# Kernel tuning notes

Hardware: AMD Instinct MI355X
Metric: run time of the kernel (lower is better)

## Reference

```python
import jax, jax.numpy as jnp
import numpy as np

ENC_DIM, DEC_DIM, ATT_DIM = 2048, 512, 512
B, N = 256, 196


def setup_inputs() -> dict:
    key = jax.random.key(0)
    ks = jax.random.split(key, 8)
    s_enc = 1.0 / np.sqrt(ENC_DIM)
    s_dec = 1.0 / np.sqrt(DEC_DIM)
    s_full = 1.0 / np.sqrt(ATT_DIM)
    return {
        "encoder_out": jax.random.normal(ks[0], (B, N, ENC_DIM), jnp.float32),
        "hidden": jax.random.normal(ks[1], (B, DEC_DIM), jnp.float32),
        "W_enc": jax.random.uniform(ks[2], (ENC_DIM, ATT_DIM), jnp.float32, -s_enc, s_enc),
        "b_enc": jax.random.uniform(ks[3], (ATT_DIM,), jnp.float32, -s_enc, s_enc),
        "W_dec": jax.random.uniform(ks[4], (DEC_DIM, ATT_DIM), jnp.float32, -s_dec, s_dec),
        "b_dec": jax.random.uniform(ks[5], (ATT_DIM,), jnp.float32, -s_dec, s_dec),
        "W_full": jax.random.uniform(ks[6], (ATT_DIM, 1), jnp.float32, -s_full, s_full),
        "b_full": jax.random.uniform(ks[7], (1,), jnp.float32, -s_full, s_full),
    }


def reference(encoder_out, hidden, W_enc, b_enc, W_dec, b_dec, W_full, b_full):
    # enc proj: [B, N, A]; dec proj: [B, 1, A] broadcast over pixels
    att1 = jnp.einsum('bne,ea->bna', encoder_out, W_enc) + b_enc
    att2 = hidden @ W_dec + b_dec                       # [B, A]
    att = jax.nn.relu(att1 + att2[:, None, :])          # [B, N, A]
    scores = (jnp.einsum('bna,a->bn', att, W_full[:, 0]) + b_full[0])  # [B, N]
    alpha = jax.nn.softmax(scores, axis=1)              # softmax over pixels
    context = jnp.einsum('bne,bn->be', encoder_out, alpha)  # [B, E]
    return (context, alpha)
```

## Files before the change

### kernel.cpp

```cpp
#include <hip/hip_runtime.h>
#include <hip/hip_bf16.h>
#include <stdint.h>

#define ENC_DIM 2048
#define ATT_DIM 512
#define BATCH   256
#define NPIX    196
#define MTOT    (BATCH*NPIX)
#define CTX_OFF (BATCH*ENC_DIM)

typedef __attribute__((ext_vector_type(8))) short  short8;
typedef __attribute__((ext_vector_type(4))) float  f32x4;

__device__ __forceinline__ unsigned short f2bf(float x) {
    union { float f; uint32_t u; } v; v.f = x;
    return (unsigned short)((v.u + 0x7FFFu + ((v.u >> 16) & 1u)) >> 16);
}

__global__ __launch_bounds__(256) void pack_wenc(const float* __restrict__ W,
                                                 unsigned short* __restrict__ Wp) {
    const int i  = blockIdx.x * 256 + threadIdx.x;
    const int n  = i & 511;
    const int kg = i >> 9;
    short8 v;
#pragma unroll
    for (int j = 0; j < 8; ++j)
        v[j] = (short)f2bf(W[(size_t)(kg * 8 + j) * 512 + n]);
    *(short8*)(Wp + (size_t)i * 8) = v;
}

__global__ __launch_bounds__(256) void att2_kernel(const float* __restrict__ hidden,
                                                   const float* __restrict__ Wdec,
                                                   const float* __restrict__ bdec,
                                                   const float* __restrict__ benc,
                                                   float* __restrict__ att2p) {
    __shared__ float h[512];
    const int b   = blockIdx.x;
    const int tid = threadIdx.x;
    h[tid]       = hidden[(size_t)b * 512 + tid];
    h[tid + 256] = hidden[(size_t)b * 512 + tid + 256];
    __syncthreads();
    float acc0 = bdec[tid]       + benc[tid];
    float acc1 = bdec[tid + 256] + benc[tid + 256];
#pragma unroll 4
    for (int k = 0; k < 512; ++k) {
        const float hk = h[k];
        acc0 = fmaf(hk, Wdec[(size_t)k * 512 + tid],       acc0);
        acc1 = fmaf(hk, Wdec[(size_t)k * 512 + tid + 256], acc1);
    }
    att2p[(size_t)b * 512 + tid]       = acc0;
    att2p[(size_t)b * 512 + tid + 256] = acc1;
}

__global__ __launch_bounds__(512) void score_kernel(const float* __restrict__ enc,
                                                    const unsigned short* __restrict__ Wp,
                                                    const float* __restrict__ att2p,
                                                    const float* __restrict__ Wfull,
                                                    float* __restrict__ scores) {
    __shared__ __align__(16) unsigned short ldsA[64 * 64];
    __shared__ __align__(16) unsigned short ldsB[8 * 512 * 8];
    __shared__ float lds_att2[2][ATT_DIM];
    __shared__ float lds_wf[ATT_DIM];
    __shared__ float lds_sc[64];

    const int tid = threadIdx.x;
    const int w   = tid >> 6;
    const int l   = tid & 63;
    const int m0  = blockIdx.x * 64;
    const int b0  = m0 / NPIX;
    const int b1  = (m0 + 63) / NPIX;

    lds_att2[0][tid] = att2p[(size_t)b0 * ATT_DIM + tid];
    lds_att2[1][tid] = att2p[(size_t)b1 * ATT_DIM + tid];
    if (tid < ATT_DIM - 512 + 512) lds_wf[tid] = Wfull[tid];
    if (tid < 64) lds_sc[tid] = 0.0f;

    f32x4 acc[4][4];
#pragma unroll
    for (int i = 0; i < 4; ++i)
#pragma unroll
        for (int j = 0; j < 4; ++j)
            acc[i][j] = (f32x4){0.f, 0.f, 0.f, 0.f};

    const int ar      = tid >> 3;
    const int akk     = (tid & 7) << 3;
    const int aslot   = (tid & 7) ^ (ar & 7);
    unsigned short* aw = ldsA + ar * 64 + aslot * 8;
    const float* abase = enc + (size_t)(m0 + ar) * ENC_DIM + akk;

    const short8* bsrc = (const short8*)Wp;
    short8*       bdst = (short8*)ldsB;

    for (int kc = 0; kc < ENC_DIM; kc += 64) {
        f32x4 f0 = *(const f32x4*)(abase + kc);
        f32x4 f1 = *(const f32x4*)(abase + kc + 4);
        short8 av;
        av[0] = (short)f2bf(f0[0]); av[1] = (short)f2bf(f0[1]);
        av[2] = (short)f2bf(f0[2]); av[3] = (short)f2bf(f0[3]);
        av[4] = (short)f2bf(f1[0]); av[5] = (short)f2bf(f1[1]);
        av[6] = (short)f2bf(f1[2]); av[7] = (short)f2bf(f1[3]);
        *(short8*)aw = av;
        const short8* bs = bsrc + (size_t)kc * 64;
#pragma unroll
        for (int it = 0; it < 8; ++it)
            bdst[it * 512 + tid] = bs[it * 512 + tid];
        __syncthreads();
#pragma unroll
        for (int ks = 0; ks < 2; ++ks) {
            const int kg = ks * 4 + (l >> 4);
            short8 af[4], bfv[4];
#pragma unroll
            for (int mf = 0; mf < 4; ++mf) {
                const int r = mf * 16 + (l & 15);
                af[mf] = *(const short8*)(ldsA + r * 64 + ((kg ^ (r & 7)) * 8));
            }
#pragma unroll
            for (int nf = 0; nf < 4; ++nf) {
                const int col = w * 64 + nf * 16 + (l & 15);
                bfv[nf] = *(const short8*)(ldsB + ((size_t)kg * 512 + col) * 8);
            }
#pragma unroll
            for (int mf = 0; mf < 4; ++mf)
#pragma unroll
                for (int nf = 0; nf < 4; ++nf)
                    acc[mf][nf] = __builtin_amdgcn_mfma_f32_16x16x32_bf16(
                        af[mf], bfv[nf], acc[mf][nf], 0, 0, 0);
        }
        __syncthreads();
    }

#pragma unroll
    for (int mf = 0; mf < 4; ++mf) {
#pragma unroll
        for (int reg = 0; reg < 4; ++reg) {
            const int row = mf * 16 + ((l >> 4) << 2) + reg;
            const int sel = ((m0 + row) >= (b0 + 1) * NPIX) ? 1 : 0;
            float sv = 0.0f;
#pragma unroll
            for (int nf = 0; nf < 4; ++nf) {
                const int col = (w << 6) + (nf << 4) + (l & 15);
                float v = acc[mf][nf][reg] + lds_att2[sel][col];
                v = fmaxf(v, 0.0f);
                sv = fmaf(v, lds_wf[col], sv);
            }
            sv += __shfl_xor(sv, 8);
            sv += __shfl_xor(sv, 4);
            sv += __shfl_xor(sv, 2);
            sv += __shfl_xor(sv, 1);
            if ((l & 15) == 0) atomicAdd(&lds_sc[row], sv);
        }
    }
    __syncthreads();
    if (tid < 64) scores[m0 + tid] = lds_sc[tid];
}

__global__ __launch_bounds__(256) void ctx_kernel(const float* __restrict__ enc,
                                                  const float* __restrict__ scores,
                                                  float* __restrict__ out) {
    __shared__ float salpha[NPIX];
    __shared__ float red[8];
    const int tid  = threadIdx.x;
    const int lane = tid & 63;
    const int wid  = tid >> 6;
    const int b    = blockIdx.x >> 1;
    const int eh   = blockIdx.x & 1;

    const float sv = (tid < NPIX) ? scores[(size_t)b * NPIX + tid] : -1e30f;
    float mx = sv;
#pragma unroll
    for (int m = 32; m >= 1; m >>= 1) mx = fmaxf(mx, __shfl_xor(mx, m));
    if (lane == 0) red[wid] = mx;
    __syncthreads();
    if (tid == 0) red[4] = fmaxf(fmaxf(red[0], red[1]), fmaxf(red[2], red[3]));
    __syncthreads();
    const float bm = red[4];
    const float ex = (tid < NPIX) ? __expf(sv - bm) : 0.0f;
    float sm = ex;
#pragma unroll
    for (int m = 32; m >= 1; m >>= 1) sm += __shfl_xor(sm, m);
    if (lane == 0) red[wid] = sm;
    __syncthreads();
    if (tid == 0) red[5] = red[0] + red[1] + red[2] + red[3];
    __syncthreads();
    const float inv = 1.0f / red[5];
    const float av  = ex * inv;
    if (tid < NPIX) {
        salpha[tid] = av;
        if (eh == 0) out[CTX_OFF + (size_t)b * NPIX + tid] = av;
    }
    __syncthreads();

    const float* ep = enc + (size_t)b * NPIX * ENC_DIM + eh * 1024 + tid;
    float a0 = 0.f, a1 = 0.f, a2 = 0.f, a3 = 0.f;
#pragma unroll 2
    for (int n = 0; n < NPIX; ++n) {
        const float al = salpha[n];
        const float* p = ep + (size_t)n * ENC_DIM;
        a0 = fmaf(al, p[0],   a0);
        a1 = fmaf(al, p[256], a1);
        a2 = fmaf(al, p[512], a2);
        a3 = fmaf(al, p[768], a3);
    }
    float* cp = out + (size_t)b * 2048 + eh * 1024 + tid;
    cp[0]   = a0;
    cp[256] = a1;
    cp[512] = a2;
    cp[768] = a3;
}

extern "C" void kernel_launch(void* const* d_in, const int* in_sizes, int n_in,
                              void* d_out, int out_size, void* d_ws, size_t ws_size,
                              hipStream_t stream) {
    const float* enc    = (const float*)d_in[0];
    const float* hidden = (const float*)d_in[1];
    const float* Wenc   = (const float*)d_in[2];
    const float* benc   = (const float*)d_in[3];
    const float* Wdec   = (const float*)d_in[4];
    const float* bdec   = (const float*)d_in[5];
    const float* Wfull  = (const float*)d_in[6];
    float* out = (float*)d_out;

    unsigned short* Wp    = (unsigned short*)d_ws;
    float*          att2p = (float*)((char*)d_ws + (2u << 20));
    float*          scores= (float*)((char*)d_ws + (2u << 20) + (512u << 10));

    pack_wenc  <<<512, 256, 0, stream>>>(Wenc, Wp);
    att2_kernel<<<BATCH, 256, 0, stream>>>(hidden, Wdec, bdec, benc, att2p);
    score_kernel<<<MTOT / 64, 512, 0, stream>>>(enc, Wp, att2p, Wfull, scores);
    ctx_kernel <<<BATCH * 2, 256, 0, stream>>>(enc, scores, out);
}
```

Baseline: 303.1 us.

## Double-buffer score GEMM with direct global-to-LDS loads and vectorize context kernel

The score GEMM now uses a K-chunk of 32 with double-buffered LDS tiles. W_enc tiles are loaded with global_load_lds directly into shared memory, and the next chunk of encoder data is prefetched while the current one runs on MFMA, so there is one barrier per chunk instead of two. The context kernel splits each batch into four 512-wide slices, uses float4 loads, and has two pixel phases reduced through LDS. Halving K per step doubles the number of barriers and iterations, and the launch_bounds hint of 4 blocks may force register spills.

```diff
diff --git a/kernel.cpp b/kernel.cpp
--- a/kernel.cpp
+++ b/kernel.cpp
@@ -8,13 +8,21 @@
 #define NPIX    196
 #define MTOT    (BATCH*NPIX)
 #define CTX_OFF (BATCH*ENC_DIM)
+#define KC      32
+#define NCHUNK  (ENC_DIM/KC)
 
 typedef __attribute__((ext_vector_type(8))) short  short8;
 typedef __attribute__((ext_vector_type(4))) float  f32x4;
 
-__device__ __forceinline__ unsigned short f2bf(float x) {
+__device__ __forceinline__ unsigned int f2bf(float x) {
     union { float f; uint32_t u; } v; v.f = x;
-    return (unsigned short)((v.u + 0x7FFFu + ((v.u >> 16) & 1u)) >> 16);
+    return (v.u + 0x7FFFu + ((v.u >> 16) & 1u)) >> 16;
+}
+
+__device__ __forceinline__ void gll16(const void* g, void* l) {
+    __builtin_amdgcn_global_load_lds(
+        (const __attribute__((address_space(1))) unsigned int*)g,
+        (__attribute__((address_space(3))) unsigned int*)l, 16, 0, 0);
 }
 
 __global__ __launch_bounds__(256) void pack_wenc(const float* __restrict__ W,
@@ -52,13 +60,13 @@
     att2p[(size_t)b * 512 + tid + 256] = acc1;
 }
 
-__global__ __launch_bounds__(512) void score_kernel(const float* __restrict__ enc,
-                                                    const unsigned short* __restrict__ Wp,
-                                                    const float* __restrict__ att2p,
-                                                    const float* __restrict__ Wfull,
-                                                    float* __restrict__ scores) {
-    __shared__ __align__(16) unsigned short ldsA[64 * 64];
-    __shared__ __align__(16) unsigned short ldsB[8 * 512 * 8];
+__global__ __launch_bounds__(512, 4) void score_kernel(const float* __restrict__ enc,
+                                                       const unsigned short* __restrict__ Wp,
+                                                       const float* __restrict__ att2p,
+                                                       const float* __restrict__ Wfull,
+                                                       float* __restrict__ scores) {
+    __shared__ __align__(16) unsigned short ldsA[2][64 * KC];
+    __shared__ __align__(16) unsigned short ldsB[2][4 * 512 * 8];
     __shared__ float lds_att2[2][ATT_DIM];
     __shared__ float lds_wf[ATT_DIM];
     __shared__ float lds_sc[64];
@@ -72,7 +80,7 @@
 
     lds_att2[0][tid] = att2p[(size_t)b0 * ATT_DIM + tid];
     lds_att2[1][tid] = att2p[(size_t)b1 * ATT_DIM + tid];
-    if (tid < ATT_DIM - 512 + 512) lds_wf[tid] = Wfull[tid];
+    lds_wf[tid] = Wfull[tid];
     if (tid < 64) lds_sc[tid] = 0.0f;
 
     f32x4 acc[4][4];
@@ -82,51 +90,81 @@
         for (int j = 0; j < 4; ++j)
             acc[i][j] = (f32x4){0.f, 0.f, 0.f, 0.f};
 
-    const int ar      = tid >> 3;
-    const int akk     = (tid & 7) << 3;
-    const int aslot   = (tid & 7) ^ (ar & 7);
-    unsigned short* aw = ldsA + ar * 64 + aslot * 8;
-    const float* abase = enc + (size_t)(m0 + ar) * ENC_DIM + akk;
-
-    const short8* bsrc = (const short8*)Wp;
-    short8*       bdst = (short8*)ldsB;
-
-    for (int kc = 0; kc < ENC_DIM; kc += 64) {
-        f32x4 f0 = *(const f32x4*)(abase + kc);
-        f32x4 f1 = *(const f32x4*)(abase + kc + 4);
-        short8 av;
-        av[0] = (short)f2bf(f0[0]); av[1] = (short)f2bf(f0[1]);
-        av[2] = (short)f2bf(f0[2]); av[3] = (short)f2bf(f0[3]);
-        av[4] = (short)f2bf(f1[0]); av[5] = (short)f2bf(f1[1]);
-        av[6] = (short)f2bf(f1[2]); av[7] = (short)f2bf(f1[3]);
-        *(short8*)aw = av;
-        const short8* bs = bsrc + (size_t)kc * 64;
-#pragma unroll
-        for (int it = 0; it < 8; ++it)
-            bdst[it * 512 + tid] = bs[it * 512 + tid];
-        __syncthreads();
-#pragma unroll
-        for (int ks = 0; ks < 2; ++ks) {
-            const int kg = ks * 4 + (l >> 4);
-            short8 af[4], bfv[4];
-#pragma unroll
-            for (int mf = 0; mf < 4; ++mf) {
-                const int r = mf * 16 + (l & 15);
-                af[mf] = *(const short8*)(ldsA + r * 64 + ((kg ^ (r & 7)) * 8));
-            }
-#pragma unroll
-            for (int nf = 0; nf < 4; ++nf) {
-                const int col = w * 64 + nf * 16 + (l & 15);
-                bfv[nf] = *(const short8*)(ldsB + ((size_t)kg * 512 + col) * 8);
-            }
-#pragma unroll
-            for (int mf = 0; mf < 4; ++mf)
-#pragma unroll
-                for (int nf = 0; nf < 4; ++nf)
-                    acc[mf][nf] = __builtin_amdgcn_mfma_f32_16x16x32_bf16(
-                        af[mf], bfv[nf], acc[mf][nf], 0, 0, 0);
+    const int ar  = tid >> 3;
+    const int ah  = tid & 7;
+    const int axr = (ar >> 1) & 3;
+    const float* aG = enc + (size_t)(m0 + ar) * ENC_DIM + ah * 4;
+    const int a_wr_off = ar * KC + ((ah >> 1) ^ axr) * 8 + (ah & 1) * 4;
+
+    const unsigned char* WpB = (const unsigned char*)Wp;
+
+    int a_rd[4], b_rd[4];
+#pragma unroll
+    for (int mf = 0; mf < 4; ++mf) {
+        const int r = mf * 16 + (l & 15);
+        a_rd[mf] = r * KC + (((l >> 4) ^ ((r >> 1) & 3)) * 8);
+    }
+#pragma unroll
+    for (int nf = 0; nf < 4; ++nf) {
+        const int col = w * 64 + nf * 16 + (l & 15);
+        b_rd[nf] = ((l >> 4) * 512 + col) * 8;
+    }
+
+#pragma unroll
+    for (int it = 0; it < 4; ++it) {
+        const int seg = w * 4 + it;
+        gll16(WpB + (size_t)seg * 1024 + l * 16,
+              (unsigned char*)ldsB[0] + seg * 1024 + l * 16);
+    }
+    {
+        f32x4 a0 = *(const f32x4*)aG;
+        uint32_t* dst = (uint32_t*)(ldsA[0] + a_wr_off);
+        dst[0] = f2bf(a0[0]) | (f2bf(a0[1]) << 16);
+        dst[1] = f2bf(a0[2]) | (f2bf(a0[3]) << 16);
+    }
+    __syncthreads();
+
+#pragma unroll 2
+    for (int c = 0; c < NCHUNK - 1; ++c) {
+        const int p = c & 1;
+#pragma unroll
+        for (int it = 0; it < 4; ++it) {
+            const int seg = w * 4 + it;
+            gll16(WpB + (size_t)(c + 1) * 32768 + seg * 1024 + l * 16,
+                  (unsigned char*)ldsB[p ^ 1] + seg * 1024 + l * 16);
+        }
+        f32x4 an = *(const f32x4*)(aG + (c + 1) * KC);
+        short8 af[4], bfv[4];
+#pragma unroll
+        for (int mf = 0; mf < 4; ++mf) af[mf]  = *(const short8*)(ldsA[p] + a_rd[mf]);
+#pragma unroll
+        for (int nf = 0; nf < 4; ++nf) bfv[nf] = *(const short8*)(ldsB[p] + b_rd[nf]);
+#pragma unroll
+        for (int mf = 0; mf < 4; ++mf)
+#pragma unroll
+            for (int nf = 0; nf < 4; ++nf)
+                acc[mf][nf] = __builtin_amdgcn_mfma_f32_16x16x32_bf16(
+                    af[mf], bfv[nf], acc[mf][nf], 0, 0, 0);
+        {
+            uint32_t* dst = (uint32_t*)(ldsA[p ^ 1] + a_wr_off);
+            dst[0] = f2bf(an[0]) | (f2bf(an[1]) << 16);
+            dst[1] = f2bf(an[2]) | (f2bf(an[3]) << 16);
         }
         __syncthreads();
+    }
+    {
+        const int p = (NCHUNK - 1) & 1;
+        short8 af[4], bfv[4];
+#pragma unroll
+        for (int mf = 0; mf < 4; ++mf) af[mf]  = *(const short8*)(ldsA[p] + a_rd[mf]);
+#pragma unroll
+        for (int nf = 0; nf < 4; ++nf) bfv[nf] = *(const short8*)(ldsB[p] + b_rd[nf]);
+#pragma unroll
+        for (int mf = 0; mf < 4; ++mf)
+#pragma unroll
+            for (int nf = 0; nf < 4; ++nf)
+                acc[mf][nf] = __builtin_amdgcn_mfma_f32_16x16x32_bf16(
+                    af[mf], bfv[nf], acc[mf][nf], 0, 0, 0);
     }
 
 #pragma unroll
@@ -159,11 +197,12 @@
                                                   float* __restrict__ out) {
     __shared__ float salpha[NPIX];
     __shared__ float red[8];
+    __shared__ float partial[512];
     const int tid  = threadIdx.x;
     const int lane = tid & 63;
     const int wid  = tid >> 6;
-    const int b    = blockIdx.x >> 1;
-    const int eh   = blockIdx.x & 1;
+    const int b    = blockIdx.x >> 2;
+    const int eq   = blockIdx.x & 3;
 
     const float sv = (tid < NPIX) ? scores[(size_t)b * NPIX + tid] : -1e30f;
     float mx = sv;
@@ -183,29 +222,29 @@
     if (tid == 0) red[5] = red[0] + red[1] + red[2] + red[3];
     __syncthreads();
     const float inv = 1.0f / red[5];
-    const float av  = ex * inv;
     if (tid < NPIX) {
+        const float av = ex * inv;
         salpha[tid] = av;
-        if (eh == 0) out[CTX_OFF + (size_t)b * NPIX + tid] = av;
-    }
-    __syncthreads();
-
-    const float* ep = enc + (size_t)b * NPIX * ENC_DIM + eh * 1024 + tid;
-    float a0 = 0.f, a1 = 0.f, a2 = 0.f, a3 = 0.f;
-#pragma unroll 2
-    for (int n = 0; n < NPIX; ++n) {
+        if (eq == 0) out[CTX_OFF + (size_t)b * NPIX + tid] = av;
+    }
+    __syncthreads();
+
+    const int l128 = tid & 127;
+    const int ph   = tid >> 7;
+    const float* ep = enc + (size_t)b * NPIX * ENC_DIM + eq * 512 + l128 * 4;
+    f32x4 acc = (f32x4){0.f, 0.f, 0.f, 0.f};
+#pragma unroll 4
+    for (int n = ph; n < NPIX; n += 2) {
         const float al = salpha[n];
-        const float* p = ep + (size_t)n * ENC_DIM;
-        a0 = fmaf(al, p[0],   a0);
-        a1 = fmaf(al, p[256], a1);
-        a2 = fmaf(al, p[512], a2);
-        a3 = fmaf(al, p[768], a3);
-    }
-    float* cp = out + (size_t)b * 2048 + eh * 1024 + tid;
-    cp[0]   = a0;
-    cp[256] = a1;
-    cp[512] = a2;
-    cp[768] = a3;
+        f32x4 v = *(const f32x4*)(ep + (size_t)n * ENC_DIM);
+        acc += v * al;
+    }
+    if (ph == 1) *(f32x4*)(partial + l128 * 4) = acc;
+    __syncthreads();
+    if (ph == 0) {
+        f32x4 o = acc + *(const f32x4*)(partial + l128 * 4);
+        *(f32x4*)(out + (size_t)b * ENC_DIM + eq * 512 + l128 * 4) = o;
+    }
 }
 
 extern "C" void kernel_launch(void* const* d_in, const int* in_sizes, int n_in,
@@ -227,5 +266,5 @@
     pack_wenc  <<<512, 256, 0, stream>>>(Wenc, Wp);
     att2_kernel<<<BATCH, 256, 0, stream>>>(hidden, Wdec, bdec, benc, att2p);
     score_kernel<<<MTOT / 64, 512, 0, stream>>>(enc, Wp, att2p, Wfull, scores);
-    ctx_kernel <<<BATCH * 2, 256, 0, stream>>>(enc, scores, out);
-}
+    ctx_kernel <<<BATCH * 4, 256, 0, stream>>>(enc, scores, out);
+}
```

Result: slower. 335.6 us (+10.7%).

## Fuse score GEMM, softmax and context into one per-batch kernel

Applied to the files above, without the earlier changes.

Replaces the separate score and context kernels with one kernel per batch element. It computes the 196 pixel scores in two 112-row sub-tiles, using double-buffered bf16 A tiles in LDS and B fragments read directly from global/L2, then does the softmax and the context reduction in the same block. This is meant to drop the scores round trip and a kernel launch, and to reuse encoder_out while it is likely still in cache. In exchange the grid shrinks to 256 blocks, which may underfill the GPU, and padded rows waste some MFMA work.

```diff
diff --git a/kernel.cpp b/kernel.cpp
--- a/kernel.cpp
+++ b/kernel.cpp
@@ -6,15 +6,19 @@
 #define ATT_DIM 512
 #define BATCH   256
 #define NPIX    196
-#define MTOT    (BATCH*NPIX)
+#define MROWS   (BATCH*NPIX)
 #define CTX_OFF (BATCH*ENC_DIM)
+#define KC      128
+#define NCH     (ENC_DIM/KC)
+#define MSUB    112
+#define ABUF    (MSUB*KC*2)
 
 typedef __attribute__((ext_vector_type(8))) short  short8;
 typedef __attribute__((ext_vector_type(4))) float  f32x4;
 
-__device__ __forceinline__ unsigned short f2bf(float x) {
+__device__ __forceinline__ uint32_t f2bf(float x) {
     union { float f; uint32_t u; } v; v.f = x;
-    return (unsigned short)((v.u + 0x7FFFu + ((v.u >> 16) & 1u)) >> 16);
+    return (v.u + 0x7FFFu + ((v.u >> 16) & 1u)) >> 16;
 }
 
 __global__ __launch_bounds__(256) void pack_wenc(const float* __restrict__ W,
@@ -52,160 +56,190 @@
     att2p[(size_t)b * 512 + tid + 256] = acc1;
 }
 
-__global__ __launch_bounds__(512) void score_kernel(const float* __restrict__ enc,
-                                                    const unsigned short* __restrict__ Wp,
-                                                    const float* __restrict__ att2p,
-                                                    const float* __restrict__ Wfull,
-                                                    float* __restrict__ scores) {
-    __shared__ __align__(16) unsigned short ldsA[64 * 64];
-    __shared__ __align__(16) unsigned short ldsB[8 * 512 * 8];
-    __shared__ float lds_att2[2][ATT_DIM];
+__global__ __launch_bounds__(512, 2) void fused_kernel(const float* __restrict__ enc,
+                                                       const unsigned short* __restrict__ Wp,
+                                                       const float* __restrict__ att2p,
+                                                       const float* __restrict__ Wfull,
+                                                       float* __restrict__ out) {
+    __shared__ __align__(16) unsigned char ldsA[2 * ABUF];
+    __shared__ float lds_att2[ATT_DIM];
     __shared__ float lds_wf[ATT_DIM];
-    __shared__ float lds_sc[64];
+    __shared__ float lds_sc[224];
+    __shared__ float salpha[NPIX];
+    __shared__ float red[16];
 
     const int tid = threadIdx.x;
     const int w   = tid >> 6;
     const int l   = tid & 63;
-    const int m0  = blockIdx.x * 64;
-    const int b0  = m0 / NPIX;
-    const int b1  = (m0 + 63) / NPIX;
-
-    lds_att2[0][tid] = att2p[(size_t)b0 * ATT_DIM + tid];
-    lds_att2[1][tid] = att2p[(size_t)b1 * ATT_DIM + tid];
-    if (tid < ATT_DIM - 512 + 512) lds_wf[tid] = Wfull[tid];
-    if (tid < 64) lds_sc[tid] = 0.0f;
-
-    f32x4 acc[4][4];
-#pragma unroll
-    for (int i = 0; i < 4; ++i)
-#pragma unroll
-        for (int j = 0; j < 4; ++j)
-            acc[i][j] = (f32x4){0.f, 0.f, 0.f, 0.f};
-
-    const int ar      = tid >> 3;
-    const int akk     = (tid & 7) << 3;
-    const int aslot   = (tid & 7) ^ (ar & 7);
-    unsigned short* aw = ldsA + ar * 64 + aslot * 8;
-    const float* abase = enc + (size_t)(m0 + ar) * ENC_DIM + akk;
-
-    const short8* bsrc = (const short8*)Wp;
-    short8*       bdst = (short8*)ldsB;
-
-    for (int kc = 0; kc < ENC_DIM; kc += 64) {
-        f32x4 f0 = *(const f32x4*)(abase + kc);
-        f32x4 f1 = *(const f32x4*)(abase + kc + 4);
-        short8 av;
-        av[0] = (short)f2bf(f0[0]); av[1] = (short)f2bf(f0[1]);
-        av[2] = (short)f2bf(f0[2]); av[3] = (short)f2bf(f0[3]);
-        av[4] = (short)f2bf(f1[0]); av[5] = (short)f2bf(f1[1]);
-        av[6] = (short)f2bf(f1[2]); av[7] = (short)f2bf(f1[3]);
-        *(short8*)aw = av;
-        const short8* bs = bsrc + (size_t)kc * 64;
-#pragma unroll
-        for (int it = 0; it < 8; ++it)
-            bdst[it * 512 + tid] = bs[it * 512 + tid];
+    const int b   = blockIdx.x;
+
+    lds_att2[tid] = att2p[(size_t)b * ATT_DIM + tid];
+    lds_wf[tid]   = Wfull[tid];
+    if (tid < 224) lds_sc[tid] = 0.0f;
+
+    int boff[4];
+#pragma unroll
+    for (int nf = 0; nf < 4; ++nf)
+        boff[nf] = (((l >> 4) * 512) + (w << 6) + (nf << 4) + (l & 15)) * 8;
+
+    const int g  = tid & 31;
+    const int rr = tid >> 5;
+    const int aoffL0 = rr * 256 + (((g >> 1) ^ (rr & 7)) << 4) + ((g & 1) << 3);
+    const int axk   = l & 7;
+    const int afrow = (l & 15) << 8;
+
+    for (int sub = 0; sub < 2; ++sub) {
+        int rowOff[7];
+#pragma unroll
+        for (int i = 0; i < 7; ++i) {
+            int grow = b * NPIX + sub * MSUB + rr + 16 * i;
+            if (grow > MROWS - 1) grow = MROWS - 1;
+            rowOff[i] = grow * ENC_DIM;
+        }
+        const float* aBase = enc + g * 4;
+
+        f32x4 acc[7][4];
+#pragma unroll
+        for (int i = 0; i < 7; ++i)
+#pragma unroll
+            for (int j = 0; j < 4; ++j)
+                acc[i][j] = (f32x4){0.f, 0.f, 0.f, 0.f};
+
+        {
+            f32x4 sA[7];
+#pragma unroll
+            for (int i = 0; i < 7; ++i) sA[i] = *(const f32x4*)(aBase + rowOff[i]);
+#pragma unroll
+            for (int i = 0; i < 7; ++i) {
+                uint2 u;
+                u.x = f2bf(sA[i][0]) | (f2bf(sA[i][1]) << 16);
+                u.y = f2bf(sA[i][2]) | (f2bf(sA[i][3]) << 16);
+                *(uint2*)(ldsA + aoffL0 + i * 4096) = u;
+            }
+        }
         __syncthreads();
-#pragma unroll
-        for (int ks = 0; ks < 2; ++ks) {
-            const int kg = ks * 4 + (l >> 4);
-            short8 af[4], bfv[4];
-#pragma unroll
-            for (int mf = 0; mf < 4; ++mf) {
-                const int r = mf * 16 + (l & 15);
-                af[mf] = *(const short8*)(ldsA + r * 64 + ((kg ^ (r & 7)) * 8));
-            }
-#pragma unroll
-            for (int nf = 0; nf < 4; ++nf) {
-                const int col = w * 64 + nf * 16 + (l & 15);
-                bfv[nf] = *(const short8*)(ldsB + ((size_t)kg * 512 + col) * 8);
-            }
-#pragma unroll
-            for (int mf = 0; mf < 4; ++mf)
+
+        for (int c = 0; c < NCH; ++c) {
+            const int p = c & 1;
+            const unsigned char* ldsR = ldsA + p * ABUF;
+            unsigned char*       ldsW = ldsA + (p ^ 1) * ABUF;
+            const bool more = (c < NCH - 1);
+
+            f32x4 sA[7];
+            if (more) {
+#pragma unroll
+                for (int i = 0; i < 7; ++i)
+                    sA[i] = *(const f32x4*)(aBase + rowOff[i] + (c + 1) * KC);
+            }
+
+            const unsigned short* bC = Wp + (size_t)c * 65536;
+            short8 bf0[8], bf1[8];
+#pragma unroll
+            for (int s2 = 0; s2 < 2; ++s2)
 #pragma unroll
                 for (int nf = 0; nf < 4; ++nf)
-                    acc[mf][nf] = __builtin_amdgcn_mfma_f32_16x16x32_bf16(
-                        af[mf], bfv[nf], acc[mf][nf], 0, 0, 0);
-        }
-        __syncthreads();
-    }
-
-#pragma unroll
-    for (int mf = 0; mf < 4; ++mf) {
-#pragma unroll
-        for (int reg = 0; reg < 4; ++reg) {
-            const int row = mf * 16 + ((l >> 4) << 2) + reg;
-            const int sel = ((m0 + row) >= (b0 + 1) * NPIX) ? 1 : 0;
-            float sv = 0.0f;
-#pragma unroll
-            for (int nf = 0; nf < 4; ++nf) {
-                const int col = (w << 6) + (nf << 4) + (l & 15);
-                float v = acc[mf][nf][reg] + lds_att2[sel][col];
-                v = fmaxf(v, 0.0f);
-                sv = fmaf(v, lds_wf[col], sv);
-            }
-            sv += __shfl_xor(sv, 8);
-            sv += __shfl_xor(sv, 4);
-            sv += __shfl_xor(sv, 2);
-            sv += __shfl_xor(sv, 1);
-            if ((l & 15) == 0) atomicAdd(&lds_sc[row], sv);
-        }
-    }
-    __syncthreads();
-    if (tid < 64) scores[m0 + tid] = lds_sc[tid];
-}
-
-__global__ __launch_bounds__(256) void ctx_kernel(const float* __restrict__ enc,
-                                                  const float* __restrict__ scores,
-                                                  float* __restrict__ out) {
-    __shared__ float salpha[NPIX];
-    __shared__ float red[8];
-    const int tid  = threadIdx.x;
-    const int lane = tid & 63;
-    const int wid  = tid >> 6;
-    const int b    = blockIdx.x >> 1;
-    const int eh   = blockIdx.x & 1;
-
-    const float sv = (tid < NPIX) ? scores[(size_t)b * NPIX + tid] : -1e30f;
-    float mx = sv;
+                    bf0[s2 * 4 + nf] = *(const short8*)(bC + boff[nf] + s2 * 16384);
+
+#define STEP(S, BARR, BASE)                                                        \
+            {                                                                      \
+                const int so = ((((S) * 4) + (l >> 4)) ^ axk) << 4;                \
+                _Pragma("unroll")                                                  \
+                for (int mf = 0; mf < 7; ++mf) {                                   \
+                    short8 af = *(const short8*)(ldsR + afrow + so + mf * 4096);   \
+                    _Pragma("unroll")                                              \
+                    for (int nf = 0; nf < 4; ++nf)                                 \
+                        acc[mf][nf] = __builtin_amdgcn_mfma_f32_16x16x32_bf16(     \
+                            af, BARR[(BASE) + nf], acc[mf][nf], 0, 0, 0);          \
+                }                                                                  \
+            }
+
+            STEP(0, bf0, 0)
+#pragma unroll
+            for (int s2 = 0; s2 < 2; ++s2)
+#pragma unroll
+                for (int nf = 0; nf < 4; ++nf)
+                    bf1[s2 * 4 + nf] = *(const short8*)(bC + boff[nf] + (2 + s2) * 16384);
+            STEP(1, bf0, 4)
+            STEP(2, bf1, 0)
+            STEP(3, bf1, 4)
+#undef STEP
+
+            if (more) {
+#pragma unroll
+                for (int i = 0; i < 7; ++i) {
+                    uint2 u;
+                    u.x = f2bf(sA[i][0]) | (f2bf(sA[i][1]) << 16);
+                    u.y = f2bf(sA[i][2]) | (f2bf(sA[i][3]) << 16);
+                    *(uint2*)(ldsW + aoffL0 + i * 4096) = u;
+                }
+            }
+            __syncthreads();
+        }
+
+#pragma unroll
+        for (int mf = 0; mf < 7; ++mf) {
+#pragma unroll
+            for (int reg = 0; reg < 4; ++reg) {
+                const int row = sub * MSUB + mf * 16 + ((l >> 4) << 2) + reg;
+                float sv = 0.0f;
+#pragma unroll
+                for (int nf = 0; nf < 4; ++nf) {
+                    const int col = (w << 6) + (nf << 4) + (l & 15);
+                    float v = acc[mf][nf][reg] + lds_att2[col];
+                    v = fmaxf(v, 0.0f);
+                    sv = fmaf(v, lds_wf[col], sv);
+                }
+                sv += __shfl_xor(sv, 8);
+                sv += __shfl_xor(sv, 4);
+                sv += __shfl_xor(sv, 2);
+                sv += __shfl_xor(sv, 1);
+                if ((l & 15) == 0 && row < NPIX) atomicAdd(&lds_sc[row], sv);
+            }
+        }
+    }
+    __syncthreads();
+
+    const float sval = (tid < NPIX) ? lds_sc[tid] : -1e30f;
+    float mx = sval;
 #pragma unroll
     for (int m = 32; m >= 1; m >>= 1) mx = fmaxf(mx, __shfl_xor(mx, m));
-    if (lane == 0) red[wid] = mx;
-    __syncthreads();
-    if (tid == 0) red[4] = fmaxf(fmaxf(red[0], red[1]), fmaxf(red[2], red[3]));
-    __syncthreads();
-    const float bm = red[4];
-    const float ex = (tid < NPIX) ? __expf(sv - bm) : 0.0f;
+    if (l == 0) red[w] = mx;
+    __syncthreads();
+    if (tid == 0) {
+        float m2 = red[0];
+#pragma unroll
+        for (int i = 1; i < 8; ++i) m2 = fmaxf(m2, red[i]);
+        red[8] = m2;
+    }
+    __syncthreads();
+    const float bm = red[8];
+    const float ex = (tid < NPIX) ? __expf(sval - bm) : 0.0f;
     float sm = ex;
 #pragma unroll
     for (int m = 32; m >= 1; m >>= 1) sm += __shfl_xor(sm, m);
-    if (lane == 0) red[wid] = sm;
-    __syncthreads();
-    if (tid == 0) red[5] = red[0] + red[1] + red[2] + red[3];
-    __syncthreads();
-    const float inv = 1.0f / red[5];
-    const float av  = ex * inv;
+    if (l == 0) red[w] = sm;
+    __syncthreads();
+    if (tid == 0) {
+        float s2 = 0.f;
+#pragma unroll
+        for (int i = 0; i < 8; ++i) s2 += red[i];
+        red[9] = s2;
+    }
+    __syncthreads();
+    const float inv = 1.0f / red[9];
     if (tid < NPIX) {
+        const float av = ex * inv;
         salpha[tid] = av;
-        if (eh == 0) out[CTX_OFF + (size_t)b * NPIX + tid] = av;
-    }
-    __syncthreads();
-
-    const float* ep = enc + (size_t)b * NPIX * ENC_DIM + eh * 1024 + tid;
-    float a0 = 0.f, a1 = 0.f, a2 = 0.f, a3 = 0.f;
-#pragma unroll 2
-    for (int n = 0; n < NPIX; ++n) {
-        const float al = salpha[n];
-        const float* p = ep + (size_t)n * ENC_DIM;
-        a0 = fmaf(al, p[0],   a0);
-        a1 = fmaf(al, p[256], a1);
-        a2 = fmaf(al, p[512], a2);
-        a3 = fmaf(al, p[768], a3);
-    }
-    float* cp = out + (size_t)b * 2048 + eh * 1024 + tid;
-    cp[0]   = a0;
-    cp[256] = a1;
-    cp[512] = a2;
-    cp[768] = a3;
+        out[CTX_OFF + (size_t)b * NPIX + tid] = av;
+    }
+    __syncthreads();
+
+    const float* ep = enc + (size_t)b * NPIX * ENC_DIM + tid * 4;
+    f32x4 a2 = (f32x4){0.f, 0.f, 0.f, 0.f};
+#pragma unroll 4
+    for (int n = 0; n < NPIX; ++n)
+        a2 += salpha[n] * *(const f32x4*)(ep + (size_t)n * ENC_DIM);
+    *(f32x4*)(out + (size_t)b * ENC_DIM + tid * 4) = a2;
 }
 
 extern "C" void kernel_launch(void* const* d_in, const int* in_sizes, int n_in,
@@ -222,10 +256,8 @@
 
     unsigned short* Wp    = (unsigned short*)d_ws;
     float*          att2p = (float*)((char*)d_ws + (2u << 20));
-    float*          scores= (float*)((char*)d_ws + (2u << 20) + (512u << 10));
-
-    pack_wenc  <<<512, 256, 0, stream>>>(Wenc, Wp);
-    att2_kernel<<<BATCH, 256, 0, stream>>>(hidden, Wdec, bdec, benc, att2p);
-    score_kernel<<<MTOT / 64, 512, 0, stream>>>(enc, Wp, att2p, Wfull, scores);
-    ctx_kernel <<<BATCH * 2, 256, 0, stream>>>(enc, scores, out);
-}
+
+    pack_wenc   <<<512, 256, 0, stream>>>(Wenc, Wp);
+    att2_kernel <<<BATCH, 256, 0, stream>>>(hidden, Wdec, bdec, benc, att2p);
+    fused_kernel<<<BATCH, 512, 0, stream>>>(enc, Wp, att2p, Wfull, out);
+}
```

Result: faster. 289.1 us (-4.6%).
